# Optimization experiments

Measured on AMD Instinct MI355X. Metric: run time of the kernel, lower is better.

The kernel has to match this reference:

```python
import jax, jax.numpy as jnp
import numpy as np

B, S, C_IN, C_OUT = 8, 2048, 512, 512

def setup_inputs() -> dict:
    key = jax.random.key(0)
    k1, k2, k3, k4 = jax.random.split(key, 4)
    sc = 1.0 / np.sqrt(C_IN)
    return {
        "x": jax.random.normal(k1, (B, S, C_IN), dtype=jnp.float32),
        "Wq": jax.random.normal(k2, (C_OUT, C_IN), dtype=jnp.float32) * sc,
        "Wk": jax.random.normal(k3, (C_OUT, C_IN), dtype=jnp.float32) * sc,
        "Wv": jax.random.normal(k4, (C_OUT, C_IN), dtype=jnp.float32) * sc,
    }

def reference(x, Wq, Wk, Wv):
    # x: [B,S,Cin]; weights [Cout,Cin] (torch Linear convention, no bias)
    C = Wq.shape[0]
    dk = jnp.sqrt(jnp.float32(1.0) / C)  # torch: sqrt(1/out_features)
    q = jnp.einsum('bsi,oi->bso', x, Wq)
    k = jnp.einsum('bsi,oi->bso', x, Wk)
    v = jnp.einsum('bsi,oi->bso', x, Wv)
    phi_q = jax.nn.elu(q * dk) + 1.0
    phi_k = jax.nn.elu(k * dk) + 1.0
    b = x.shape[0]
    mem0 = jnp.zeros((b, C, C), x.dtype)   # running sum of phi_k v^T
    zeta0 = jnp.zeros((b, C), x.dtype)     # running sum of phi_k
    def step(carry, inp):
        mem, zeta = carry
        pq, pk, vv = inp                    # each [B,C]
        dm = pk[:, :, None] * vv[:, None, :]              # [B,C,C]
        scale = jnp.einsum('bc,bc->b', pq, pk + zeta) + 1e-5
        num = jnp.einsum('bc,bcd->bd', pq, dm + mem)
        y = num / scale[:, None]
        # state updates are under torch.no_grad -> detach
        new_mem = jax.lax.stop_gradient(mem + dm)
        new_zeta = jax.lax.stop_gradient(zeta + pk)
        return (new_mem, new_zeta), y
    xs = (phi_q.transpose(1, 0, 2), phi_k.transpose(1, 0, 2), v.transpose(1, 0, 2))
    _, ys = jax.lax.scan(step, (mem0, zeta0), xs)  # ys: [S,B,C]
    return ys.transpose(1, 0, 2)                   # [B,S,C]
```

## Files before the change

kernel.cpp:

```cpp
#include <hip/hip_runtime.h>


constexpr int Bn  = 8;
constexpr int Sn  = 2048;
constexpr int Cn  = 512;
constexpr int Tn  = 128;
constexpr int NCn = 16;
constexpr float DKf = 0.04419417382415922f;

typedef __attribute__((ext_vector_type(8))) short bf16x8;
typedef __attribute__((ext_vector_type(4))) float f32x4;

__device__ __forceinline__ unsigned short f2bf(float f) {
  unsigned u = __float_as_uint(f);
  u = (u + 0x7fffu + ((u >> 16) & 1u)) >> 16;
  return (unsigned short)u;
}
__device__ __forceinline__ float bf2f(unsigned short h) {
  return __uint_as_float(((unsigned)h) << 16);
}
__device__ __forceinline__ float phi_f(float u) {
  float s = u * DKf;
  return s > 0.0f ? s + 1.0f : __expf(s);
}

__device__ __forceinline__ void stage128x32(const unsigned short* __restrict__ g,
                                            int ld, unsigned short* lds,
                                            int wid, int lane) {
#pragma unroll
  for (int cc = 0; cc < 2; ++cc) {
    const int row = cc * 64 + wid * 16 + (lane >> 2);
    const int ks  = (lane & 3) ^ ((row >> 1) & 3);
    const unsigned short* src = g + (size_t)row * ld + ks * 8;
    unsigned short* dst = lds + (size_t)(cc * 256 + wid * 64) * 8;
    __builtin_amdgcn_global_load_lds(
        (const __attribute__((address_space(1))) void*)src,
        (__attribute__((address_space(3))) void*)dst, 16, 0, 0);
  }
}

__device__ __forceinline__ void mm_loop(const unsigned short* __restrict__ Ag, int lda,
                                        const unsigned short* __restrict__ Bg, int ldb,
                                        int nkt,
                                        unsigned short* Al, unsigned short* Bl,
                                        f32x4 acc[4][4]) {
  const int t = threadIdx.x, wid = t >> 6, lane = t & 63;
  const int wm = wid >> 1, wn = wid & 1;
  const int fr = lane & 15, kb = lane >> 4;
  stage128x32(Ag, lda, Al, wid, lane);
  stage128x32(Bg, ldb, Bl, wid, lane);
  if (nkt > 1) {
    stage128x32(Ag + 32, lda, Al + 4096, wid, lane);
    stage128x32(Bg + 32, ldb, Bl + 4096, wid, lane);
  }
  int cur = 0;
  for (int kt = 0; kt < nkt; ++kt) {
    if (kt + 2 < nkt) {
      const int nx2 = (cur + 2 >= 3) ? cur - 1 : cur + 2;
      stage128x32(Ag + (kt + 2) * 32, lda, Al + nx2 * 4096, wid, lane);
      stage128x32(Bg + (kt + 2) * 32, ldb, Bl + nx2 * 4096, wid, lane);
      asm volatile("s_waitcnt vmcnt(8)" ::: "memory");
    } else if (kt + 1 < nkt) {
      asm volatile("s_waitcnt vmcnt(4)" ::: "memory");
    } else {
      asm volatile("s_waitcnt vmcnt(0)" ::: "memory");
    }
    __builtin_amdgcn_s_barrier();
    asm volatile("" ::: "memory");
    const unsigned short* Ac = Al + cur * 4096;
    const unsigned short* Bc = Bl + cur * 4096;
    bf16x8 af[4], bf[4];
#pragma unroll
    for (int m = 0; m < 4; ++m) {
      const int r = wm * 64 + m * 16 + fr;
      af[m] = *(const bf16x8*)&Ac[r * 32 + ((kb ^ ((r >> 1) & 3)) << 3)];
    }
#pragma unroll
    for (int n = 0; n < 4; ++n) {
      const int r = wn * 64 + n * 16 + fr;
      bf[n] = *(const bf16x8*)&Bc[r * 32 + ((kb ^ ((r >> 1) & 3)) << 3)];
    }
#pragma unroll
    for (int m = 0; m < 4; ++m)
#pragma unroll
      for (int n = 0; n < 4; ++n)
        acc[m][n] = __builtin_amdgcn_mfma_f32_16x16x32_bf16(af[m], bf[n], acc[m][n], 0, 0, 0);
    __builtin_amdgcn_s_barrier();
    asm volatile("" ::: "memory");
    cur = (cur + 1 >= 3) ? 0 : cur + 1;
  }
}

__global__ __launch_bounds__(256) void k_cast_x(const float* __restrict__ x,
                                                unsigned short* __restrict__ xb) {
  const size_t i8 = ((size_t)blockIdx.x * 256 + threadIdx.x) * 8;
  float4 a = *(const float4*)&x[i8];
  float4 b = *(const float4*)&x[i8 + 4];
  uint4 o;
  o.x = (unsigned)f2bf(a.x) | ((unsigned)f2bf(a.y) << 16);
  o.y = (unsigned)f2bf(a.z) | ((unsigned)f2bf(a.w) << 16);
  o.z = (unsigned)f2bf(b.x) | ((unsigned)f2bf(b.y) << 16);
  o.w = (unsigned)f2bf(b.z) | ((unsigned)f2bf(b.w) << 16);
  *(uint4*)&xb[i8] = o;
}

__global__ __launch_bounds__(256) void k_cast_w(const float* __restrict__ Wq,
                                                const float* __restrict__ Wk,
                                                const float* __restrict__ Wv,
                                                unsigned short* __restrict__ Wb) {
  const int z = blockIdx.y;
  const float* __restrict__ src = (z == 0) ? Wq : (z == 1 ? Wk : Wv);
  const size_t i8 = ((size_t)blockIdx.x * 256 + threadIdx.x) * 8;
  float4 a = *(const float4*)&src[i8];
  float4 b = *(const float4*)&src[i8 + 4];
  uint4 o;
  o.x = (unsigned)f2bf(a.x) | ((unsigned)f2bf(a.y) << 16);
  o.y = (unsigned)f2bf(a.z) | ((unsigned)f2bf(a.w) << 16);
  o.z = (unsigned)f2bf(b.x) | ((unsigned)f2bf(b.y) << 16);
  o.w = (unsigned)f2bf(b.z) | ((unsigned)f2bf(b.w) << 16);
  *(uint4*)&Wb[(size_t)z * Cn * Cn + i8] = o;
}

__global__ __launch_bounds__(256) void k_proj(
    const unsigned short* __restrict__ xb, const unsigned short* __restrict__ Wb,
    unsigned short* __restrict__ PQ, unsigned short* __restrict__ PK,
    unsigned short* __restrict__ PKt, unsigned short* __restrict__ Vt,
    float* __restrict__ zsum)
{
  __shared__ unsigned short Al[3 * 128 * 32], Bl[3 * 128 * 32];
  __shared__ float zbuf[2][128];
  const int bid = blockIdx.x;
  const int xcd = bid & 7, idx = bid >> 3;
  const int n = idx & 3, z = (idx >> 2) % 3, mloc = idx / 12;
  const int n0 = n * 128, m0 = (xcd * 16 + mloc) * 128;
  const int t = threadIdx.x, wid = t >> 6, lane = t & 63;
  const int wm = wid >> 1, wn = wid & 1;
  f32x4 acc[4][4];
  const f32x4 zero = {0.f, 0.f, 0.f, 0.f};
#pragma unroll
  for (int m = 0; m < 4; ++m)
#pragma unroll
    for (int nn = 0; nn < 4; ++nn) acc[m][nn] = zero;

  mm_loop(xb + (size_t)m0 * Cn, Cn,
          Wb + (size_t)z * Cn * Cn + (size_t)n0 * Cn, Cn, Cn / 32, Al, Bl, acc);

  float ps[4] = {0.f, 0.f, 0.f, 0.f};
#pragma unroll
  for (int m = 0; m < 4; ++m)
#pragma unroll
    for (int nn = 0; nn < 4; ++nn) {
      const int row0 = m0 + wm * 64 + m * 16 + ((lane >> 4) << 2);
      const int col  = n0 + wn * 64 + nn * 16 + (lane & 15);
      f32x4 v = acc[m][nn];
      if (z == 0) {
#pragma unroll
        for (int j = 0; j < 4; ++j)
          PQ[(size_t)(row0 + j) * Cn + col] = f2bf(phi_f(v[j]));
      } else if (z == 1) {
        ushort4 p;
#pragma unroll
        for (int j = 0; j < 4; ++j) {
          unsigned short u = f2bf(phi_f(v[j]));
          PK[(size_t)(row0 + j) * Cn + col] = u;
          (&p.x)[j] = u;
          ps[nn] += bf2f(u);
        }
        const int b = row0 >> 11, tq = row0 & (Sn - 1);
        *(ushort4*)&PKt[((size_t)b * Cn + col) * Sn + tq] = p;
      } else {
        ushort4 p;
#pragma unroll
        for (int j = 0; j < 4; ++j) (&p.x)[j] = f2bf(v[j]);
        const int b = row0 >> 11, tq = row0 & (Sn - 1);
        *(ushort4*)&Vt[((size_t)b * Cn + col) * Sn + tq] = p;
      }
    }

  if (z == 1) {
#pragma unroll
    for (int nn = 0; nn < 4; ++nn) {
      float v = ps[nn];
      v += __shfl_xor(v, 16); v += __shfl_xor(v, 32);
      if (lane < 16) zbuf[wm][wn * 64 + nn * 16 + lane] = v;
    }
    __syncthreads();
    if (t < 128) {
      const int b = m0 >> 11, ch = (m0 >> 7) & 15;
      zsum[((size_t)b * NCn + ch) * Cn + n0 + t] = zbuf[0][t] + zbuf[1][t];
    }
  }
}

__global__ __launch_bounds__(256) void k_gram(
    const unsigned short* __restrict__ PQ, const unsigned short* __restrict__ PK,
    const float* __restrict__ zsum,
    unsigned short* __restrict__ Abuf, float* __restrict__ scale)
{
  __shared__ unsigned short Al[3 * 128 * 32], Bl[3 * 128 * 32];
  __shared__ float rsmem[2][128];
  __shared__ float zpl[512];
  const int b = blockIdx.y, ch = blockIdx.x;
  const size_t base = ((size_t)b * Sn + ch * Tn) * Cn;
  f32x4 acc[4][4];
  const f32x4 zero = {0.f, 0.f, 0.f, 0.f};
#pragma unroll
  for (int m = 0; m < 4; ++m)
#pragma unroll
    for (int n = 0; n < 4; ++n) acc[m][n] = zero;

  mm_loop(PQ + base, Cn, PK + base, Cn, Cn / 32, Al, Bl, acc);

  const int t = threadIdx.x, wid = t >> 6, lane = t & 63;
  const int wm = wid >> 1, wn = wid & 1;
  float rsum[4][4];
#pragma unroll
  for (int m = 0; m < 4; ++m)
#pragma unroll
    for (int j = 0; j < 4; ++j) rsum[m][j] = 0.f;
#pragma unroll
  for (int m = 0; m < 4; ++m)
#pragma unroll
    for (int n = 0; n < 4; ++n) {
      f32x4 v = acc[m][n];
#pragma unroll
      for (int j = 0; j < 4; ++j) {
        const int row = wm * 64 + m * 16 + ((lane >> 4) << 2) + j;
        const int col = wn * 64 + n * 16 + (lane & 15);
        unsigned short u = (col <= row) ? f2bf(v[j]) : 0;
        Abuf[((size_t)(b * NCn + ch) * Tn + row) * Tn + col] = u;
        rsum[m][j] += bf2f(u);
      }
    }
#pragma unroll
  for (int m = 0; m < 4; ++m)
#pragma unroll
    for (int j = 0; j < 4; ++j) {
      float r = rsum[m][j];
      r += __shfl_xor(r, 1); r += __shfl_xor(r, 2);
      r += __shfl_xor(r, 4); r += __shfl_xor(r, 8);
      if ((lane & 15) == 0)
        rsmem[wn][wm * 64 + m * 16 + ((lane >> 4) << 2) + j] = r;
    }
#pragma unroll
  for (int e = 0; e < 2; ++e) {
    const int c = t + e * 256;
    float s = 0.f;
    for (int ch2 = 0; ch2 < ch; ++ch2)
      s += zsum[((size_t)b * NCn + ch2) * Cn + c];
    zpl[c] = s;
  }
  __syncthreads();
  const int row = t >> 1, half = (t & 1) * 256;
  const unsigned short* pq = PQ + base + (size_t)row * Cn + half;
  float dacc = 0.f;
  for (int i = 0; i < 256; i += 8) {
    uint4 q = *(const uint4*)(pq + i);
    dacc += bf2f((unsigned short)(q.x & 0xffff)) * zpl[half + i + 0]
          + bf2f((unsigned short)(q.x >> 16))    * zpl[half + i + 1]
          + bf2f((unsigned short)(q.y & 0xffff)) * zpl[half + i + 2]
          + bf2f((unsigned short)(q.y >> 16))    * zpl[half + i + 3]
          + bf2f((unsigned short)(q.z & 0xffff)) * zpl[half + i + 4]
          + bf2f((unsigned short)(q.z >> 16))    * zpl[half + i + 5]
          + bf2f((unsigned short)(q.w & 0xffff)) * zpl[half + i + 6]
          + bf2f((unsigned short)(q.w >> 16))    * zpl[half + i + 7];
  }
  dacc += __shfl_xor(dacc, 1);
  if ((t & 1) == 0)
    scale[(size_t)b * Sn + ch * Tn + row] =
        rsmem[0][row] + rsmem[1][row] + dacc + 1e-5f;
}

__device__ __forceinline__ void stage64x128(const unsigned short* __restrict__ g,
                                            int ld, unsigned short* lds,
                                            int wid, int lane) {
#pragma unroll
  for (int i = 0; i < 4; ++i) {
    const int row = wid * 16 + i * 4 + (lane >> 4);
    const int s   = (lane & 15) ^ (row & 7);
    const unsigned short* src = g + (size_t)row * ld + s * 8;
    unsigned short* dst = lds + (size_t)(wid * 16 + i * 4) * 128;
    __builtin_amdgcn_global_load_lds(
        (const __attribute__((address_space(1))) void*)src,
        (__attribute__((address_space(3))) void*)dst, 16, 0, 0);
  }
}

__global__ __launch_bounds__(256) void k_kvp(
    const unsigned short* __restrict__ PKt, const unsigned short* __restrict__ Vt,
    unsigned short* __restrict__ Mpre)
{
  __shared__ unsigned short Al[2 * 64 * 128], Bl[2 * 64 * 128];
  const int bid = blockIdx.x;
  const int b = bid & 7, idx = bid >> 3;
  const int d0 = (idx & 7) * 64, c0 = (idx >> 3) * 64;
  const int t = threadIdx.x, wid = t >> 6, lane = t & 63;
  const int wm = wid >> 1, wn = wid & 1;
  const int fr = lane & 15, kb = lane >> 4;
  f32x4 acc[2][2];
  const f32x4 zero = {0.f, 0.f, 0.f, 0.f};
#pragma unroll
  for (int m = 0; m < 2; ++m)
#pragma unroll
    for (int n = 0; n < 2; ++n) acc[m][n] = zero;
  const unsigned short* Ag = PKt + ((size_t)b * Cn + c0) * Sn;
  const unsigned short* Bg = Vt  + ((size_t)b * Cn + d0) * Sn;
  stage64x128(Ag, Sn, Al, wid, lane);
  stage64x128(Bg, Sn, Bl, wid, lane);
  int cur = 0;
  for (int ch = 0; ch < NCn; ++ch) {
    const int nxt = cur ^ 1;
    if (ch + 1 < NCn) {
      stage64x128(Ag + (ch + 1) * Tn, Sn, Al + nxt * 8192, wid, lane);
      stage64x128(Bg + (ch + 1) * Tn, Sn, Bl + nxt * 8192, wid, lane);
      asm volatile("s_waitcnt vmcnt(8)" ::: "memory");
    } else {
      asm volatile("s_waitcnt vmcnt(0)" ::: "memory");
    }
    __builtin_amdgcn_s_barrier();
    asm volatile("" ::: "memory");
    if (ch > 0) {
#pragma unroll
      for (int m = 0; m < 2; ++m)
#pragma unroll
        for (int n = 0; n < 2; ++n) {
          const int c_row = c0 + wm * 32 + m * 16 + (kb << 2);
          const int d     = d0 + wn * 32 + n * 16 + fr;
          ushort4 p;
#pragma unroll
          for (int j = 0; j < 4; ++j) (&p.x)[j] = f2bf(acc[m][n][j]);
          *(ushort4*)&Mpre[((size_t)(b * NCn + ch) * Cn + d) * Cn + c_row] = p;
        }
    }
    const unsigned short* Ac = Al + cur * 8192;
    const unsigned short* Bc = Bl + cur * 8192;
#pragma unroll
    for (int kt = 0; kt < 4; ++kt) {
      bf16x8 af[2], bf[2];
#pragma unroll
      for (int m = 0; m < 2; ++m) {
        const int r = wm * 32 + m * 16 + fr;
        af[m] = *(const bf16x8*)&Ac[r * 128 + (((kt * 4 + kb) ^ (r & 7)) << 3)];
      }
#pragma unroll
      for (int n = 0; n < 2; ++n) {
        const int r = wn * 32 + n * 16 + fr;
        bf[n] = *(const bf16x8*)&Bc[r * 128 + (((kt * 4 + kb) ^ (r & 7)) << 3)];
      }
#pragma unroll
      for (int m = 0; m < 2; ++m)
#pragma unroll
        for (int n = 0; n < 2; ++n)
          acc[m][n] = __builtin_amdgcn_mfma_f32_16x16x32_bf16(af[m], bf[n], acc[m][n], 0, 0, 0);
    }
    __builtin_amdgcn_s_barrier();
    asm volatile("" ::: "memory");
    cur = nxt;
  }
}

__global__ __launch_bounds__(256) void k_avinter(
    const unsigned short* __restrict__ Abuf, const unsigned short* __restrict__ Vt,
    const unsigned short* __restrict__ PQ, const unsigned short* __restrict__ Mpre,
    const float* __restrict__ scale, float* __restrict__ out)
{
  __shared__ unsigned short Al[3 * 128 * 32], Bl[3 * 128 * 32];
  const int bid = blockIdx.x;
  const int logical = (bid & 7) * 64 + (bid >> 3);
  const int d0 = (logical & 3) * 128;
  const int ch = (logical >> 2) & 15;
  const int b  = logical >> 6;
  const int t0 = ch * Tn;
  f32x4 acc[4][4];
  const f32x4 zero = {0.f, 0.f, 0.f, 0.f};
#pragma unroll
  for (int m = 0; m < 4; ++m)
#pragma unroll
    for (int n = 0; n < 4; ++n) acc[m][n] = zero;

  mm_loop(Abuf + (size_t)(b * NCn + ch) * Tn * Tn, Tn,
          Vt + ((size_t)b * Cn + d0) * Sn + t0, Sn, Tn / 32, Al, Bl, acc);
  if (ch > 0)
    mm_loop(PQ + ((size_t)b * Sn + t0) * Cn, Cn,
            Mpre + ((size_t)(b * NCn + ch) * Cn + d0) * Cn, Cn, Cn / 32, Al, Bl, acc);

  const int t = threadIdx.x, wid = t >> 6, lane = t & 63;
  const int wm = wid >> 1, wn = wid & 1;
#pragma unroll
  for (int m = 0; m < 4; ++m)
#pragma unroll
    for (int n = 0; n < 4; ++n) {
      const int row0 = t0 + wm * 64 + m * 16 + ((lane >> 4) << 2);
      const int col  = d0 + wn * 64 + n * 16 + (lane & 15);
      f32x4 v = acc[m][n];
#pragma unroll
      for (int j = 0; j < 4; ++j) {
        const size_t sidx = (size_t)b * Sn + row0 + j;
        out[sidx * Cn + col] = v[j] / scale[sidx];
      }
    }
}

extern "C" void kernel_launch(void* const* d_in, const int* in_sizes, int n_in,
                              void* d_out, int out_size, void* d_ws, size_t ws_size,
                              hipStream_t stream)
{
  const float* x  = (const float*)d_in[0];
  const float* Wq = (const float*)d_in[1];
  const float* Wk = (const float*)d_in[2];
  const float* Wv = (const float*)d_in[3];
  float* out = (float*)d_out;

  unsigned short* xb   = (unsigned short*)d_ws;
  unsigned short* Wb   = xb   + (size_t)Bn * Sn * Cn;
  unsigned short* PQ   = Wb   + (size_t)3 * Cn * Cn;
  unsigned short* PK   = PQ   + (size_t)Bn * Sn * Cn;
  unsigned short* PKt  = PK   + (size_t)Bn * Sn * Cn;
  unsigned short* Vt   = PKt  + (size_t)Bn * Sn * Cn;
  unsigned short* Abuf = Vt   + (size_t)Bn * Sn * Cn;
  unsigned short* Mpre = Abuf + (size_t)Bn * NCn * Tn * Tn;
  float* scale = (float*)(Mpre + (size_t)Bn * NCn * Cn * Cn);
  float* zsum  = scale + (size_t)Bn * Sn;
  (void)ws_size; (void)in_sizes; (void)n_in; (void)out_size;

  hipLaunchKernelGGL(k_cast_x, dim3(4096), dim3(256), 0, stream, x, xb);
  hipLaunchKernelGGL(k_cast_w, dim3(128, 3), dim3(256), 0, stream, Wq, Wk, Wv, Wb);
  hipLaunchKernelGGL(k_proj, dim3(1536), dim3(256), 0, stream, xb, Wb, PQ, PK, PKt, Vt, zsum);
  hipLaunchKernelGGL(k_gram, dim3(NCn, Bn), dim3(256), 0, stream, PQ, PK, zsum, Abuf, scale);
  hipLaunchKernelGGL(k_kvp, dim3(512), dim3(256), 0, stream, PKt, Vt, Mpre);
  hipLaunchKernelGGL(k_avinter, dim3(512), dim3(256), 0, stream, Abuf, Vt, PQ, Mpre, scale, out);
}
```

Measured before the change: 132.2 us.

## Stage transposed PKt/Vt/Mpre stores through LDS and raise MFMA wave priority

k_proj no longer writes PKt and Vt directly with scattered 8-byte stores that stride by the sequence length. It writes the tile transposed into LDS, reusing the GEMM staging buffers, and then emits coalesced 16-byte row stores. k_kvp does the same for Mpre through a small padded LDS tile, at the cost of an extra barrier per chunk. s_setprio is also raised around the MFMA blocks in both GEMM loops so math waves get issue priority over loading waves. The trade is extra LDS traffic and synchronization in exchange for far fewer uncoalesced global write transactions.

```diff
diff --git a/kernel.cpp b/kernel.cpp
--- a/kernel.cpp
+++ b/kernel.cpp
@@ -80,11 +80,13 @@
       const int r = wn * 64 + n * 16 + fr;
       bf[n] = *(const bf16x8*)&Bc[r * 32 + ((kb ^ ((r >> 1) & 3)) << 3)];
     }
+    __builtin_amdgcn_s_setprio(1);
 #pragma unroll
     for (int m = 0; m < 4; ++m)
 #pragma unroll
       for (int n = 0; n < 4; ++n)
         acc[m][n] = __builtin_amdgcn_mfma_f32_16x16x32_bf16(af[m], bf[n], acc[m][n], 0, 0, 0);
+    __builtin_amdgcn_s_setprio(0);
     __builtin_amdgcn_s_barrier();
     asm volatile("" ::: "memory");
     cur = (cur + 1 >= 3) ? 0 : cur + 1;
@@ -127,8 +129,11 @@
     unsigned short* __restrict__ PKt, unsigned short* __restrict__ Vt,
     float* __restrict__ zsum)
 {
-  __shared__ unsigned short Al[3 * 128 * 32], Bl[3 * 128 * 32];
+  __shared__ unsigned short smem[2 * 3 * 128 * 32];
   __shared__ float zbuf[2][128];
+  unsigned short* Al = smem;
+  unsigned short* Bl = smem + 3 * 4096;
+  unsigned short* Tt = smem;
   const int bid = blockIdx.x;
   const int xcd = bid & 7, idx = bid >> 3;
   const int n = idx & 3, z = (idx >> 2) % 3, mloc = idx / 12;
@@ -150,8 +155,10 @@
   for (int m = 0; m < 4; ++m)
 #pragma unroll
     for (int nn = 0; nn < 4; ++nn) {
-      const int row0 = m0 + wm * 64 + m * 16 + ((lane >> 4) << 2);
-      const int col  = n0 + wn * 64 + nn * 16 + (lane & 15);
+      const int rl0 = wm * 64 + m * 16 + ((lane >> 4) << 2);
+      const int cl  = wn * 64 + nn * 16 + (lane & 15);
+      const int row0 = m0 + rl0;
+      const int col  = n0 + cl;
       f32x4 v = acc[m][nn];
       if (z == 0) {
 #pragma unroll
@@ -166,14 +173,12 @@
           (&p.x)[j] = u;
           ps[nn] += bf2f(u);
         }
-        const int b = row0 >> 11, tq = row0 & (Sn - 1);
-        *(ushort4*)&PKt[((size_t)b * Cn + col) * Sn + tq] = p;
+        *(ushort4*)&Tt[cl * 136 + rl0] = p;
       } else {
         ushort4 p;
 #pragma unroll
         for (int j = 0; j < 4; ++j) (&p.x)[j] = f2bf(v[j]);
-        const int b = row0 >> 11, tq = row0 & (Sn - 1);
-        *(ushort4*)&Vt[((size_t)b * Cn + col) * Sn + tq] = p;
+        *(ushort4*)&Tt[cl * 136 + rl0] = p;
       }
     }
 
@@ -184,10 +189,22 @@
       v += __shfl_xor(v, 16); v += __shfl_xor(v, 32);
       if (lane < 16) zbuf[wm][wn * 64 + nn * 16 + lane] = v;
     }
+  }
+  if (z >= 1) {
     __syncthreads();
-    if (t < 128) {
+    if (z == 1 && t < 128) {
       const int b = m0 >> 11, ch = (m0 >> 7) & 15;
       zsum[((size_t)b * NCn + ch) * Cn + n0 + t] = zbuf[0][t] + zbuf[1][t];
+    }
+    const int c = t & 127, seg = t >> 7;
+    const int bI = m0 >> 11, tq0 = m0 & (Sn - 1);
+    unsigned short* dstT = (z == 1 ? PKt : Vt)
+                         + ((size_t)bI * Cn + n0 + c) * Sn + tq0 + seg * 64;
+    const unsigned short* srcT = &Tt[c * 136 + seg * 64];
+#pragma unroll
+    for (int i = 0; i < 8; ++i) {
+      const int cc = ((i ^ (c & 7)) << 3);
+      *(uint4*)(dstT + cc) = *(const uint4*)(srcT + cc);
     }
   }
 }
@@ -290,7 +307,10 @@
     const unsigned short* __restrict__ PKt, const unsigned short* __restrict__ Vt,
     unsigned short* __restrict__ Mpre)
 {
-  __shared__ unsigned short Al[2 * 64 * 128], Bl[2 * 64 * 128];
+  __shared__ unsigned short smem[2 * 8192 * 2 + 64 * 72];
+  unsigned short* Al = smem;
+  unsigned short* Bl = smem + 2 * 8192;
+  unsigned short* T2 = smem + 4 * 8192;
   const int bid = blockIdx.x;
   const int b = bid & 7, idx = bid >> 3;
   const int d0 = (idx & 7) * 64, c0 = (idx >> 3) * 64;
@@ -324,16 +344,26 @@
       for (int m = 0; m < 2; ++m)
 #pragma unroll
         for (int n = 0; n < 2; ++n) {
-          const int c_row = c0 + wm * 32 + m * 16 + (kb << 2);
-          const int d     = d0 + wn * 32 + n * 16 + fr;
+          const int cl = wm * 32 + m * 16 + (kb << 2);
+          const int dl = wn * 32 + n * 16 + fr;
           ushort4 p;
 #pragma unroll
           for (int j = 0; j < 4; ++j) (&p.x)[j] = f2bf(acc[m][n][j]);
-          *(ushort4*)&Mpre[((size_t)(b * NCn + ch) * Cn + d) * Cn + c_row] = p;
+          *(ushort4*)&T2[dl * 72 + cl] = p;
         }
+      asm volatile("s_waitcnt lgkmcnt(0)" ::: "memory");
+      __builtin_amdgcn_s_barrier();
+      asm volatile("" ::: "memory");
+      const int r = t & 63, seg = t >> 6;
+      const unsigned short* srcT = &T2[r * 72 + seg * 16];
+      unsigned short* dstT = Mpre + ((size_t)(b * NCn + ch) * Cn + d0 + r) * Cn
+                           + c0 + seg * 16;
+      *(uint4*)dstT       = *(const uint4*)srcT;
+      *(uint4*)(dstT + 8) = *(const uint4*)(srcT + 8);
     }
     const unsigned short* Ac = Al + cur * 8192;
     const unsigned short* Bc = Bl + cur * 8192;
+    __builtin_amdgcn_s_setprio(1);
 #pragma unroll
     for (int kt = 0; kt < 4; ++kt) {
       bf16x8 af[2], bf[2];
@@ -353,6 +383,7 @@
         for (int n = 0; n < 2; ++n)
           acc[m][n] = __builtin_amdgcn_mfma_f32_16x16x32_bf16(af[m], bf[n], acc[m][n], 0, 0, 0);
     }
+    __builtin_amdgcn_s_setprio(0);
     __builtin_amdgcn_s_barrier();
     asm volatile("" ::: "memory");
     cur = nxt;
```

Measured after the change: 138.1 us. 4.5% more time.
